# Kernel optimization log

Measured on AMD Instinct MI355X. Metric: run time of the kernel, lower is better.

The kernel has to match this reference:

```python
import jax, jax.numpy as jnp
import numpy as np

N = 16384
D_IN = 1024
UNITS = 1024


def setup_inputs() -> dict:
    key = jax.random.key(0)
    ks = jax.random.split(key, 14)
    inp = {}
    inp["X"] = jax.random.normal(ks[0], (N, D_IN), dtype=jnp.float32)
    inp["S"] = jax.random.normal(ks[1], (N, UNITS), dtype=jnp.float32)
    # random_normal initializer in keras defaults to stddev=0.05
    std = 0.05
    names_U = ["Uz", "Ug", "Ur", "Uh"]
    names_W = ["Wz", "Wg", "Wr", "Wh"]
    names_b = ["bz", "bg", "br", "bh"]
    for i, n in enumerate(names_U):
        inp[n] = std * jax.random.normal(ks[2 + i], (D_IN, UNITS), dtype=jnp.float32)
    for i, n in enumerate(names_W):
        inp[n] = std * jax.random.normal(ks[6 + i], (UNITS, UNITS), dtype=jnp.float32)
    for i, n in enumerate(names_b):
        inp[n] = std * jax.random.normal(ks[10 + i], (UNITS,), dtype=jnp.float32)
    return inp


def reference(X, S, Uz, Ug, Ur, Uh, Wz, Wg, Wr, Wh, bz, bg, br, bh):
    trans = jnp.tanh
    # Fuse Z/G/R gates: concatenate U and W weights into single GEMMs.
    U_zgr = jnp.concatenate([Uz, Ug, Ur], axis=1)   # [d_in, 3*units]
    W_zgr = jnp.concatenate([Wz, Wg, Wr], axis=1)   # [units, 3*units]
    b_zgr = jnp.concatenate([bz, bg, br], axis=0)   # [3*units]
    zgr = trans(X @ U_zgr + S @ W_zgr + b_zgr)      # [N, 3*units]
    Z, G, R = jnp.split(zgr, 3, axis=1)
    # H gate depends on R via (S * R) @ Wh
    H = trans(X @ Uh + (S * R) @ Wh + bh)
    S_new = (1.0 - G) * H + Z * S
    return S_new
```

## Files before the change

### kernel.cpp

```cpp
#include <hip/hip_runtime.h>
#include <hip/hip_bf16.h>

typedef short short8 __attribute__((ext_vector_type(8)));
typedef float f32x4 __attribute__((ext_vector_type(4)));

#define NROWS 16384
#define UNITS 1024

__device__ __forceinline__ unsigned short f2bf(float x) {
    union { float f; unsigned int u; } v; v.f = x;
    unsigned int r = v.u + 0x7fffu + ((v.u >> 16) & 1u);
    return (unsigned short)(r >> 16);
}
__device__ __forceinline__ float bf2f(unsigned short h) {
    union { unsigned int u; float f; } v; v.u = ((unsigned int)h) << 16; return v.f;
}

struct TrArgs {
    const float* src[8];
    unsigned short* dh[8];
    unsigned short* dl[8];
};

__global__ void transpose_split(TrArgs args) {
    __shared__ float t[32][33];
    const float* src = args.src[blockIdx.z];
    unsigned short* dh = args.dh[blockIdx.z];
    unsigned short* dl = args.dl[blockIdx.z];
    const int tx = threadIdx.x, ty = threadIdx.y;
    const int bk = blockIdx.y * 32, bn = blockIdx.x * 32;
#pragma unroll
    for (int q = 0; q < 4; ++q)
        t[ty + q * 8][tx] = src[(size_t)(bk + ty + q * 8) * UNITS + bn + tx];
    __syncthreads();
#pragma unroll
    for (int q = 0; q < 4; ++q) {
        float v = t[tx][ty + q * 8];
        unsigned short h = f2bf(v);
        size_t o = (size_t)(bn + ty + q * 8) * UNITS + bk + tx;
        dh[o] = h;
        dl[o] = f2bf(v - bf2f(h));
    }
}

struct GArgs {
    const float* A0;
    const float* A1;
    const unsigned short* B0h; const unsigned short* B0l;
    const unsigned short* B1h; const unsigned short* B1l;
};

template <int EPI>
__global__ __launch_bounds__(256) void gemm_hl(
    GArgs g, const float* __restrict__ Sin,
    const float* __restrict__ bias0, const float* __restrict__ bias1, const float* __restrict__ bias2,
    float* __restrict__ outZ,
    float* __restrict__ Gws, float* __restrict__ SR) {
    __shared__ __align__(16) unsigned short Ah[128][64];
    __shared__ __align__(16) unsigned short Al[128][64];
    __shared__ __align__(16) unsigned short Bh[128][64];
    __shared__ __align__(16) unsigned short Bl[128][64];
    const int tid = threadIdx.x;
    const int wave = tid >> 6, lane = tid & 63;
    const int row0 = blockIdx.y * 128;
    const int col0 = blockIdx.x * 128;

    f32x4 acc[4][4] = {};

    const int arow = tid >> 4;
    const int acol = (tid & 15) * 4;
    const int brow = lane >> 3;
    const int bcol = (lane & 7) * 8;
    const int frow = lane & 15;
    const int fk = (lane >> 4) * 8;
    const int wr = (wave >> 1) * 64;
    const int wc = (wave & 1) * 64;

    for (int t = 0; t < 32; ++t) {
        const int half = t >> 4;
        const int k0 = (t & 15) * 64;
        const float* Ag = (half ? g.A1 : g.A0) + (size_t)row0 * 1024 + k0;
        const unsigned short* Bgh = (half ? g.B1h : g.B0h) + (size_t)col0 * 1024 + k0;
        const unsigned short* Bgl = (half ? g.B1l : g.B0l) + (size_t)col0 * 1024 + k0;

        float4 av[8];
#pragma unroll
        for (int l = 0; l < 8; ++l)
            av[l] = *reinterpret_cast<const float4*>(Ag + (size_t)(l * 16 + arow) * 1024 + acol);
#pragma unroll
        for (int q = 0; q < 4; ++q) {
            const int c = wave * 4 + q;
            const int r = c * 8 + brow;
            __builtin_amdgcn_global_load_lds(
                (const __attribute__((address_space(1))) unsigned int*)(Bgh + (size_t)r * 1024 + bcol),
                (__attribute__((address_space(3))) unsigned int*)((char*)&Bh[0][0] + c * 1024), 16, 0, 0);
            __builtin_amdgcn_global_load_lds(
                (const __attribute__((address_space(1))) unsigned int*)(Bgl + (size_t)r * 1024 + bcol),
                (__attribute__((address_space(3))) unsigned int*)((char*)&Bl[0][0] + c * 1024), 16, 0, 0);
        }
#pragma unroll
        for (int l = 0; l < 8; ++l) {
            const int r = l * 16 + arow;
            float4 v = av[l];
            ushort4 h, lo;
            h.x = f2bf(v.x); lo.x = f2bf(v.x - bf2f(h.x));
            h.y = f2bf(v.y); lo.y = f2bf(v.y - bf2f(h.y));
            h.z = f2bf(v.z); lo.z = f2bf(v.z - bf2f(h.z));
            h.w = f2bf(v.w); lo.w = f2bf(v.w - bf2f(h.w));
            *reinterpret_cast<ushort4*>(&Ah[r][acol]) = h;
            *reinterpret_cast<ushort4*>(&Al[r][acol]) = lo;
        }
        __syncthreads();
#pragma unroll
        for (int kk = 0; kk < 2; ++kk) {
            short8 fah[4], fal[4], fbh[4], fbl[4];
#pragma unroll
            for (int m = 0; m < 4; ++m) {
                fah[m] = *reinterpret_cast<const short8*>(&Ah[wr + m * 16 + frow][kk * 32 + fk]);
                fal[m] = *reinterpret_cast<const short8*>(&Al[wr + m * 16 + frow][kk * 32 + fk]);
            }
#pragma unroll
            for (int n = 0; n < 4; ++n) {
                fbh[n] = *reinterpret_cast<const short8*>(&Bh[wc + n * 16 + frow][kk * 32 + fk]);
                fbl[n] = *reinterpret_cast<const short8*>(&Bl[wc + n * 16 + frow][kk * 32 + fk]);
            }
#pragma unroll
            for (int m = 0; m < 4; ++m)
#pragma unroll
                for (int n = 0; n < 4; ++n) {
                    acc[m][n] = __builtin_amdgcn_mfma_f32_16x16x32_bf16(fah[m], fbh[n], acc[m][n], 0, 0, 0);
                    acc[m][n] = __builtin_amdgcn_mfma_f32_16x16x32_bf16(fal[m], fbh[n], acc[m][n], 0, 0, 0);
                    acc[m][n] = __builtin_amdgcn_mfma_f32_16x16x32_bf16(fah[m], fbl[n], acc[m][n], 0, 0, 0);
                }
        }
        __syncthreads();
    }

#pragma unroll
    for (int m = 0; m < 4; ++m)
#pragma unroll
        for (int n = 0; n < 4; ++n)
#pragma unroll
            for (int j = 0; j < 4; ++j) {
                const int row = row0 + wr + m * 16 + (lane >> 4) * 4 + j;
                const int col = col0 + wc + n * 16 + (lane & 15);
                float v = acc[m][n][j];
                if (EPI == 1) {
                    const int gate = col >> 10;
                    const int c = col & 1023;
                    const size_t ix = (size_t)row * UNITS + c;
                    if (gate == 0) {
                        outZ[ix] = tanhf(v + bias0[c]);
                    } else if (gate == 1) {
                        Gws[ix] = tanhf(v + bias1[c]);
                    } else {
                        SR[ix] = Sin[ix] * tanhf(v + bias2[c]);
                    }
                } else {
                    const size_t ix = (size_t)row * UNITS + col;
                    float h = tanhf(v + bias0[col]);
                    float z = outZ[ix];
                    float gg = Gws[ix];
                    float s = Sin[ix];
                    outZ[ix] = (1.0f - gg) * h + z * s;
                }
            }
}

extern "C" void kernel_launch(void* const* d_in, const int* in_sizes, int n_in,
                              void* d_out, int out_size, void* d_ws, size_t ws_size,
                              hipStream_t stream) {
    const float* X  = (const float*)d_in[0];
    const float* S  = (const float*)d_in[1];
    const float* Uz = (const float*)d_in[2];
    const float* Ug = (const float*)d_in[3];
    const float* Ur = (const float*)d_in[4];
    const float* Uh = (const float*)d_in[5];
    const float* Wz = (const float*)d_in[6];
    const float* Wg = (const float*)d_in[7];
    const float* Wr = (const float*)d_in[8];
    const float* Wh = (const float*)d_in[9];
    const float* bz = (const float*)d_in[10];
    const float* bg = (const float*)d_in[11];
    const float* br = (const float*)d_in[12];
    const float* bh = (const float*)d_in[13];
    float* out = (float*)d_out;

    const size_t SZ_PLANE = (size_t)NROWS * UNITS * 4;
    const size_t SZ_W3 = (size_t)3072 * 1024 * 2;
    const size_t SZ_W1 = (size_t)1024 * 1024 * 2;
    const size_t need = 2 * SZ_PLANE + 4 * SZ_W3 + 4 * SZ_W1;
    if (ws_size < need) return;

    char* w = (char*)d_ws;
    float* SR = (float*)w;          w += SZ_PLANE;
    float* G  = (float*)w;          w += SZ_PLANE;
    unsigned short* BTU_h  = (unsigned short*)w; w += SZ_W3;
    unsigned short* BTU_l  = (unsigned short*)w; w += SZ_W3;
    unsigned short* BTW_h  = (unsigned short*)w; w += SZ_W3;
    unsigned short* BTW_l  = (unsigned short*)w; w += SZ_W3;
    unsigned short* BTUh_h = (unsigned short*)w; w += SZ_W1;
    unsigned short* BTUh_l = (unsigned short*)w; w += SZ_W1;
    unsigned short* BTWh_h = (unsigned short*)w; w += SZ_W1;
    unsigned short* BTWh_l = (unsigned short*)w; w += SZ_W1;

    TrArgs ta;
    const size_t seg = (size_t)1024 * 1024;
    ta.src[0] = Uz; ta.dh[0] = BTU_h;            ta.dl[0] = BTU_l;
    ta.src[1] = Ug; ta.dh[1] = BTU_h + seg;      ta.dl[1] = BTU_l + seg;
    ta.src[2] = Ur; ta.dh[2] = BTU_h + 2 * seg;  ta.dl[2] = BTU_l + 2 * seg;
    ta.src[3] = Wz; ta.dh[3] = BTW_h;            ta.dl[3] = BTW_l;
    ta.src[4] = Wg; ta.dh[4] = BTW_h + seg;      ta.dl[4] = BTW_l + seg;
    ta.src[5] = Wr; ta.dh[5] = BTW_h + 2 * seg;  ta.dl[5] = BTW_l + 2 * seg;
    ta.src[6] = Uh; ta.dh[6] = BTUh_h;           ta.dl[6] = BTUh_l;
    ta.src[7] = Wh; ta.dh[7] = BTWh_h;           ta.dl[7] = BTWh_l;
    transpose_split<<<dim3(32, 32, 8), dim3(32, 8), 0, stream>>>(ta);

    GArgs g1;
    g1.A0 = X; g1.A1 = S;
    g1.B0h = BTU_h; g1.B0l = BTU_l; g1.B1h = BTW_h; g1.B1l = BTW_l;
    gemm_hl<1><<<dim3(24, 128), 256, 0, stream>>>(g1, S, bz, bg, br, out, G, SR);

    GArgs g2;
    g2.A0 = X; g2.A1 = SR;
    g2.B0h = BTUh_h; g2.B0l = BTUh_l; g2.B1h = BTWh_h; g2.B1l = BTWh_l;
    gemm_hl<2><<<dim3(8, 128), 256, 0, stream>>>(g2, S, bh, nullptr, nullptr, out, G, SR);
}
```

Baseline: 1.255 ms.

## Rewrite split-bf16 GEMMs with 256x256 tiles, swizzled LDS and double-buffered pipeline

```diff
diff --git a/kernel.cpp b/kernel.cpp
--- a/kernel.cpp
+++ b/kernel.cpp
@@ -2,6 +2,7 @@
 #include <hip/hip_bf16.h>
 
 typedef short short8 __attribute__((ext_vector_type(8)));
+typedef unsigned short ushort8 __attribute__((ext_vector_type(8)));
 typedef float f32x4 __attribute__((ext_vector_type(4)));
 
 #define NROWS 16384
@@ -43,122 +44,183 @@
     }
 }
 
-struct GArgs {
-    const float* A0;
-    const float* A1;
-    const unsigned short* B0h; const unsigned short* B0l;
-    const unsigned short* B1h; const unsigned short* B1l;
-};
+__global__ void img_perm_k(const unsigned short* __restrict__ BT0h, const unsigned short* __restrict__ BT0l,
+                           const unsigned short* __restrict__ BT1h, const unsigned short* __restrict__ BT1l,
+                           unsigned short* __restrict__ imgH, unsigned short* __restrict__ imgL) {
+    const int g = blockIdx.x * blockDim.x + threadIdx.x;
+    const int tile = g >> 10;
+    const int c = (g >> 2) & 255;
+    const int qp = g & 3;
+    const int cb = tile >> 6, kt = tile & 63;
+    const int col = cb * 256 + c;
+    const int kin = (qp ^ ((c >> 1) & 3)) * 8;
+    const unsigned short* sh;
+    const unsigned short* sl;
+    int k0;
+    if (kt < 32) { sh = BT0h; sl = BT0l; k0 = kt * 32; }
+    else         { sh = BT1h; sl = BT1l; k0 = (kt - 32) * 32; }
+    const size_t so = (size_t)col * 1024 + k0 + kin;
+    *reinterpret_cast<ushort8*>(imgH + (size_t)g * 8) = *reinterpret_cast<const ushort8*>(sh + so);
+    *reinterpret_cast<ushort8*>(imgL + (size_t)g * 8) = *reinterpret_cast<const ushort8*>(sl + so);
+}
 
 template <int EPI>
-__global__ __launch_bounds__(256) void gemm_hl(
-    GArgs g, const float* __restrict__ Sin,
-    const float* __restrict__ bias0, const float* __restrict__ bias1, const float* __restrict__ bias2,
-    float* __restrict__ outZ,
-    float* __restrict__ Gws, float* __restrict__ SR) {
-    __shared__ __align__(16) unsigned short Ah[128][64];
-    __shared__ __align__(16) unsigned short Al[128][64];
-    __shared__ __align__(16) unsigned short Bh[128][64];
-    __shared__ __align__(16) unsigned short Bl[128][64];
+__global__ __launch_bounds__(512, 2) void gemm8(
+    const float* __restrict__ A0, const float* __restrict__ A1,
+    const unsigned short* __restrict__ imgH, const unsigned short* __restrict__ imgL,
+    const float* __restrict__ Sin,
+    const float* __restrict__ b0, const float* __restrict__ b1, const float* __restrict__ b2,
+    float* __restrict__ outZ, float* __restrict__ Gws, float* __restrict__ SR) {
+    __shared__ __align__(16) char lds[131072];
+
     const int tid = threadIdx.x;
     const int wave = tid >> 6, lane = tid & 63;
-    const int row0 = blockIdx.y * 128;
-    const int col0 = blockIdx.x * 128;
-
-    f32x4 acc[4][4] = {};
-
-    const int arow = tid >> 4;
-    const int acol = (tid & 15) * 4;
-    const int brow = lane >> 3;
-    const int bcol = (lane & 7) * 8;
-    const int frow = lane & 15;
-    const int fk = (lane >> 4) * 8;
-    const int wr = (wave >> 1) * 64;
-    const int wc = (wave & 1) * 64;
-
-    for (int t = 0; t < 32; ++t) {
-        const int half = t >> 4;
-        const int k0 = (t & 15) * 64;
-        const float* Ag = (half ? g.A1 : g.A0) + (size_t)row0 * 1024 + k0;
-        const unsigned short* Bgh = (half ? g.B1h : g.B0h) + (size_t)col0 * 1024 + k0;
-        const unsigned short* Bgl = (half ? g.B1l : g.B0l) + (size_t)col0 * 1024 + k0;
-
-        float4 av[8];
-#pragma unroll
-        for (int l = 0; l < 8; ++l)
-            av[l] = *reinterpret_cast<const float4*>(Ag + (size_t)(l * 16 + arow) * 1024 + acol);
-#pragma unroll
-        for (int q = 0; q < 4; ++q) {
-            const int c = wave * 4 + q;
-            const int r = c * 8 + brow;
+    const int wM = wave >> 2, wN = wave & 3;
+    const int fr = lane & 15, fq = lane >> 4;
+    const int sA = ((fq ^ ((fr >> 1) & 3)) << 4);
+    const int arow = tid >> 1, ahalf = tid & 1;
+    const int awsz = (tid >> 2) & 3;
+
+    const int nwg = gridDim.x;
+    const int w = (blockIdx.x & 7) * (nwg >> 3) + (blockIdx.x >> 3);
+    const int cb = w >> 6;
+    const int rb = w & 63;
+    const int row0 = rb * 256;
+    const int col0 = cb * 256;
+
+    f32x4 acc[8][4] = {};
+    float4 av[4];
+
+    auto issueA = [&](int ts) {
+        const float* Ag = (ts < 32 ? A0 : A1) + (size_t)(row0 + arow) * 1024 + (ts & 31) * 32 + ahalf * 16;
+        av[0] = *reinterpret_cast<const float4*>(Ag);
+        av[1] = *reinterpret_cast<const float4*>(Ag + 4);
+        av[2] = *reinterpret_cast<const float4*>(Ag + 8);
+        av[3] = *reinterpret_cast<const float4*>(Ag + 12);
+    };
+    auto issueB = [&](int ts, int buf, int pl) {
+        const unsigned short* img = (pl ? imgL : imgH) + ((size_t)(cb * 64 + ts)) * 8192;
+#pragma unroll
+        for (int i = 0; i < 2; ++i) {
+            const unsigned short* src = img + (wave * 2 + i) * 512 + lane * 8;
+            char* dst = lds + (buf << 16) + 32768 + pl * 16384 + (wave * 2 + i) * 1024;
             __builtin_amdgcn_global_load_lds(
-                (const __attribute__((address_space(1))) unsigned int*)(Bgh + (size_t)r * 1024 + bcol),
-                (__attribute__((address_space(3))) unsigned int*)((char*)&Bh[0][0] + c * 1024), 16, 0, 0);
-            __builtin_amdgcn_global_load_lds(
-                (const __attribute__((address_space(1))) unsigned int*)(Bgl + (size_t)r * 1024 + bcol),
-                (__attribute__((address_space(3))) unsigned int*)((char*)&Bl[0][0] + c * 1024), 16, 0, 0);
-        }
-#pragma unroll
-        for (int l = 0; l < 8; ++l) {
-            const int r = l * 16 + arow;
-            float4 v = av[l];
-            ushort4 h, lo;
-            h.x = f2bf(v.x); lo.x = f2bf(v.x - bf2f(h.x));
-            h.y = f2bf(v.y); lo.y = f2bf(v.y - bf2f(h.y));
-            h.z = f2bf(v.z); lo.z = f2bf(v.z - bf2f(h.z));
-            h.w = f2bf(v.w); lo.w = f2bf(v.w - bf2f(h.w));
-            *reinterpret_cast<ushort4*>(&Ah[r][acol]) = h;
-            *reinterpret_cast<ushort4*>(&Al[r][acol]) = lo;
-        }
-        __syncthreads();
-#pragma unroll
-        for (int kk = 0; kk < 2; ++kk) {
-            short8 fah[4], fal[4], fbh[4], fbl[4];
-#pragma unroll
-            for (int m = 0; m < 4; ++m) {
-                fah[m] = *reinterpret_cast<const short8*>(&Ah[wr + m * 16 + frow][kk * 32 + fk]);
-                fal[m] = *reinterpret_cast<const short8*>(&Al[wr + m * 16 + frow][kk * 32 + fk]);
-            }
-#pragma unroll
-            for (int n = 0; n < 4; ++n) {
-                fbh[n] = *reinterpret_cast<const short8*>(&Bh[wc + n * 16 + frow][kk * 32 + fk]);
-                fbl[n] = *reinterpret_cast<const short8*>(&Bl[wc + n * 16 + frow][kk * 32 + fk]);
-            }
-#pragma unroll
-            for (int m = 0; m < 4; ++m)
-#pragma unroll
-                for (int n = 0; n < 4; ++n) {
-                    acc[m][n] = __builtin_amdgcn_mfma_f32_16x16x32_bf16(fah[m], fbh[n], acc[m][n], 0, 0, 0);
-                    acc[m][n] = __builtin_amdgcn_mfma_f32_16x16x32_bf16(fal[m], fbh[n], acc[m][n], 0, 0, 0);
-                    acc[m][n] = __builtin_amdgcn_mfma_f32_16x16x32_bf16(fah[m], fbl[n], acc[m][n], 0, 0, 0);
+                (const __attribute__((address_space(1))) unsigned int*)src,
+                (__attribute__((address_space(3))) unsigned int*)dst, 16, 0, 0);
+        }
+    };
+    auto writeA = [&](int buf) {
+        ushort8 h0, h1, l0, l1;
+#pragma unroll
+        for (int j = 0; j < 2; ++j) {
+            float4 v = av[j];
+            h0[j * 4 + 0] = f2bf(v.x); l0[j * 4 + 0] = f2bf(v.x - bf2f(h0[j * 4 + 0]));
+            h0[j * 4 + 1] = f2bf(v.y); l0[j * 4 + 1] = f2bf(v.y - bf2f(h0[j * 4 + 1]));
+            h0[j * 4 + 2] = f2bf(v.z); l0[j * 4 + 2] = f2bf(v.z - bf2f(h0[j * 4 + 2]));
+            h0[j * 4 + 3] = f2bf(v.w); l0[j * 4 + 3] = f2bf(v.w - bf2f(h0[j * 4 + 3]));
+        }
+#pragma unroll
+        for (int j = 0; j < 2; ++j) {
+            float4 v = av[2 + j];
+            h1[j * 4 + 0] = f2bf(v.x); l1[j * 4 + 0] = f2bf(v.x - bf2f(h1[j * 4 + 0]));
+            h1[j * 4 + 1] = f2bf(v.y); l1[j * 4 + 1] = f2bf(v.y - bf2f(h1[j * 4 + 1]));
+            h1[j * 4 + 2] = f2bf(v.z); l1[j * 4 + 2] = f2bf(v.z - bf2f(h1[j * 4 + 2]));
+            h1[j * 4 + 3] = f2bf(v.w); l1[j * 4 + 3] = f2bf(v.w - bf2f(h1[j * 4 + 3]));
+        }
+        const int q0 = (2 * ahalf) ^ awsz;
+        const int q1 = (2 * ahalf + 1) ^ awsz;
+        char* db = lds + (buf << 16) + arow * 64;
+        *reinterpret_cast<ushort8*>(db + (q0 << 4)) = h0;
+        *reinterpret_cast<ushort8*>(db + (q1 << 4)) = h1;
+        *reinterpret_cast<ushort8*>(db + 16384 + (q0 << 4)) = l0;
+        *reinterpret_cast<ushort8*>(db + 16384 + (q1 << 4)) = l1;
+    };
+
+    issueA(0);
+    issueB(0, 0, 0);
+    issueB(0, 0, 1);
+    asm volatile("s_waitcnt vmcnt(4)" ::: "memory");
+    writeA(0);
+    issueA(1);
+    asm volatile("s_waitcnt vmcnt(4) lgkmcnt(0)" ::: "memory");
+    __builtin_amdgcn_s_barrier();
+
+    for (int t = 0; t < 64; ++t) {
+        const int cur = t & 1, nxt = cur ^ 1;
+        const int tp1 = (t + 1 < 64) ? t + 1 : 0;
+        const int tp2 = (t + 2 < 64) ? t + 2 : 0;
+        const char* base = lds + (cur << 16);
+#pragma unroll
+        for (int p = 0; p < 4; ++p) {
+            const int mh = p >> 1, nh = p & 1;
+            short8 fah[4], fal[4], fbh[2], fbl[2];
+#pragma unroll
+            for (int mi = 0; mi < 4; ++mi) {
+                const int off = (wM * 128 + (mh * 4 + mi) * 16 + fr) * 64 + sA;
+                fah[mi] = *reinterpret_cast<const short8*>(base + off);
+                fal[mi] = *reinterpret_cast<const short8*>(base + 16384 + off);
+            }
+#pragma unroll
+            for (int ni = 0; ni < 2; ++ni) {
+                const int off = (wN * 64 + (nh * 2 + ni) * 16 + fr) * 64 + sA;
+                fbh[ni] = *reinterpret_cast<const short8*>(base + 32768 + off);
+                fbl[ni] = *reinterpret_cast<const short8*>(base + 49152 + off);
+            }
+            if (p == 0) issueB(tp1, nxt, 0);
+            if (p == 1) issueB(tp1, nxt, 1);
+            if (p == 2) {
+                asm volatile("s_waitcnt vmcnt(4)" ::: "memory");
+                writeA(nxt);
+            }
+            if (p == 3) issueA(tp2);
+
+            __builtin_amdgcn_s_barrier();
+            asm volatile("s_waitcnt lgkmcnt(0)" ::: "memory");
+            __builtin_amdgcn_sched_barrier(0);
+            __builtin_amdgcn_s_setprio(1);
+#pragma unroll
+            for (int mi = 0; mi < 4; ++mi)
+#pragma unroll
+                for (int ni = 0; ni < 2; ++ni) {
+                    f32x4 a = acc[mh * 4 + mi][nh * 2 + ni];
+                    a = __builtin_amdgcn_mfma_f32_16x16x32_bf16(fah[mi], fbh[ni], a, 0, 0, 0);
+                    a = __builtin_amdgcn_mfma_f32_16x16x32_bf16(fal[mi], fbh[ni], a, 0, 0, 0);
+                    a = __builtin_amdgcn_mfma_f32_16x16x32_bf16(fah[mi], fbl[ni], a, 0, 0, 0);
+                    acc[mh * 4 + mi][nh * 2 + ni] = a;
                 }
-        }
-        __syncthreads();
+            __builtin_amdgcn_s_setprio(0);
+            if (p < 3) {
+                __builtin_amdgcn_s_barrier();
+            } else {
+                asm volatile("s_waitcnt vmcnt(4) lgkmcnt(0)" ::: "memory");
+                __builtin_amdgcn_s_barrier();
+            }
+        }
     }
 
 #pragma unroll
-    for (int m = 0; m < 4; ++m)
+    for (int m = 0; m < 8; ++m)
 #pragma unroll
         for (int n = 0; n < 4; ++n)
 #pragma unroll
             for (int j = 0; j < 4; ++j) {
-                const int row = row0 + wr + m * 16 + (lane >> 4) * 4 + j;
-                const int col = col0 + wc + n * 16 + (lane & 15);
+                const int row = row0 + wM * 128 + m * 16 + (lane >> 4) * 4 + j;
+                const int col = col0 + wN * 64 + n * 16 + (lane & 15);
                 float v = acc[m][n][j];
                 if (EPI == 1) {
                     const int gate = col >> 10;
                     const int c = col & 1023;
                     const size_t ix = (size_t)row * UNITS + c;
                     if (gate == 0) {
-                        outZ[ix] = tanhf(v + bias0[c]);
+                        outZ[ix] = tanhf(v + b0[c]);
                     } else if (gate == 1) {
-                        Gws[ix] = tanhf(v + bias1[c]);
+                        Gws[ix] = tanhf(v + b1[c]);
                     } else {
-                        SR[ix] = Sin[ix] * tanhf(v + bias2[c]);
+                        SR[ix] = Sin[ix] * tanhf(v + b2[c]);
                     }
                 } else {
                     const size_t ix = (size_t)row * UNITS + col;
-                    float h = tanhf(v + bias0[col]);
+                    float h = tanhf(v + b0[col]);
                     float z = outZ[ix];
                     float gg = Gws[ix];
                     float s = Sin[ix];
@@ -187,22 +249,30 @@
     float* out = (float*)d_out;
 
     const size_t SZ_PLANE = (size_t)NROWS * UNITS * 4;
-    const size_t SZ_W3 = (size_t)3072 * 1024 * 2;
-    const size_t SZ_W1 = (size_t)1024 * 1024 * 2;
-    const size_t need = 2 * SZ_PLANE + 4 * SZ_W3 + 4 * SZ_W1;
+    const size_t SZ_IMG1 = (size_t)12 * 64 * 8192 * 2;
+    const size_t SZ_IMG2 = (size_t)4 * 64 * 8192 * 2;
+    const size_t need = 2 * SZ_PLANE + 2 * SZ_IMG1 + 2 * SZ_IMG2;
     if (ws_size < need) return;
 
-    char* w = (char*)d_ws;
-    float* SR = (float*)w;          w += SZ_PLANE;
-    float* G  = (float*)w;          w += SZ_PLANE;
-    unsigned short* BTU_h  = (unsigned short*)w; w += SZ_W3;
-    unsigned short* BTU_l  = (unsigned short*)w; w += SZ_W3;
-    unsigned short* BTW_h  = (unsigned short*)w; w += SZ_W3;
-    unsigned short* BTW_l  = (unsigned short*)w; w += SZ_W3;
-    unsigned short* BTUh_h = (unsigned short*)w; w += SZ_W1;
-    unsigned short* BTUh_l = (unsigned short*)w; w += SZ_W1;
-    unsigned short* BTWh_h = (unsigned short*)w; w += SZ_W1;
-    unsigned short* BTWh_l = (unsigned short*)w; w += SZ_W1;
+    char* wp = (char*)d_ws;
+    float* SR = (float*)wp;  wp += SZ_PLANE;
+    float* G  = (float*)wp;  wp += SZ_PLANE;
+    unsigned short* img1H = (unsigned short*)wp; wp += SZ_IMG1;
+    unsigned short* img1L = (unsigned short*)wp; wp += SZ_IMG1;
+    unsigned short* img2H = (unsigned short*)wp; wp += SZ_IMG2;
+    unsigned short* img2L = (unsigned short*)wp; wp += SZ_IMG2;
+
+    char* sc = (char*)SR;
+    const size_t W3 = (size_t)3072 * 1024 * 2;
+    const size_t W1 = (size_t)1024 * 1024 * 2;
+    unsigned short* BTU_h  = (unsigned short*)(sc);
+    unsigned short* BTU_l  = (unsigned short*)(sc + W3);
+    unsigned short* BTW_h  = (unsigned short*)(sc + 2 * W3);
+    unsigned short* BTW_l  = (unsigned short*)(sc + 3 * W3);
+    unsigned short* BTUh_h = (unsigned short*)(sc + 4 * W3);
+    unsigned short* BTUh_l = (unsigned short*)(sc + 4 * W3 + W1);
+    unsigned short* BTWh_h = (unsigned short*)(sc + 4 * W3 + 2 * W1);
+    unsigned short* BTWh_l = (unsigned short*)(sc + 4 * W3 + 3 * W1);
 
     TrArgs ta;
     const size_t seg = (size_t)1024 * 1024;
@@ -216,13 +286,9 @@
     ta.src[7] = Wh; ta.dh[7] = BTWh_h;           ta.dl[7] = BTWh_l;
     transpose_split<<<dim3(32, 32, 8), dim3(32, 8), 0, stream>>>(ta);
 
-    GArgs g1;
-    g1.A0 = X; g1.A1 = S;
-    g1.B0h = BTU_h; g1.B0l = BTU_l; g1.B1h = BTW_h; g1.B1l = BTW_l;
-    gemm_hl<1><<<dim3(24, 128), 256, 0, stream>>>(g1, S, bz, bg, br, out, G, SR);
-
-    GArgs g2;
-    g2.A0 = X; g2.A1 = SR;
-    g2.B0h = BTUh_h; g2.B0l = BTUh_l; g2.B1h = BTWh_h; g2.B1l = BTWh_l;
-    gemm_hl<2><<<dim3(8, 128), 256, 0, stream>>>(g2, S, bh, nullptr, nullptr, out, G, SR);
-}
+    img_perm_k<<<3072, 256, 0, stream>>>(BTU_h, BTU_l, BTW_h, BTW_l, img1H, img1L);
+    img_perm_k<<<1024, 256, 0, stream>>>(BTUh_h, BTUh_l, BTWh_h, BTWh_l, img2H, img2L);
+
+    gemm8<1><<<768, 512, 0, stream>>>(X, S, img1H, img1L, S, bz, bg, br, out, G, SR);
+    gemm8<2><<<256, 512, 0, stream>>>(X, SR, img2H, img2L, S, bh, nullptr, nullptr, out, G, SR);
+}
```

Result: faster. 1.121 ms (-10.7%).
